# Performance work log

Hardware: AMD Instinct MI355X
Metric: run time of the kernel (lower is better)

The kernel has to match this reference:

```python
import jax, jax.numpy as jnp
import numpy as np

NUM_GROUPS = 32
EPS = 1e-5


def group_norm(x, scale, bias):
    # x: [B, C, L], normalize per (group, batch) over (C//G, L)
    B, C, L = x.shape
    G = NUM_GROUPS
    xg = x.reshape(B, G, C // G, L)
    mean = xg.mean(axis=(2, 3), keepdims=True)
    var = xg.var(axis=(2, 3), keepdims=True)
    xg = (xg - mean) * jax.lax.rsqrt(var + EPS)
    h = xg.reshape(B, C, L)
    return h * scale[None, :, None] + bias[None, :, None]


def setup_inputs() -> dict:
    key = jax.random.key(0)
    ks = jax.random.split(key, 8)
    B, C, L = 8, 512, 2048
    s = 1.0 / np.sqrt(C)
    return {
        "x": jax.random.normal(ks[0], (B, C, L), jnp.float32),
        "gn_scale": jnp.ones((C,), jnp.float32),
        "gn_bias": jnp.zeros((C,), jnp.float32),
        "wq": jax.random.normal(ks[1], (C, C), jnp.float32) * s,
        "bq": jnp.zeros((C,), jnp.float32),
        "wk": jax.random.normal(ks[2], (C, C), jnp.float32) * s,
        "bk": jnp.zeros((C,), jnp.float32),
        "wv": jax.random.normal(ks[3], (C, C), jnp.float32) * s,
        "bv": jnp.zeros((C,), jnp.float32),
        "wo": jax.random.normal(ks[4], (C, C), jnp.float32) * s,
        "bo": jnp.zeros((C,), jnp.float32),
    }


def reference(x, gn_scale, gn_bias, wq, bq, wk, bk, wv, bv, wo, bo):
    B, C, L = x.shape
    h = group_norm(x, gn_scale, gn_bias)  # [B, C, L]
    # 1x1 conv == per-position linear; produce [B, L, C] directly
    q = jnp.einsum('oc,bcl->blo', wq, h) + bq
    k = jnp.einsum('oc,bcl->blo', wk, h) + bk
    v = jnp.einsum('oc,bcl->blo', wv, h) + bv
    scale = jnp.asarray(C, x.dtype) ** -0.5
    w = jnp.einsum('bqc,bkc->bqk', q, k) * scale  # [B, L, L]
    w = jax.nn.softmax(w, axis=-1)
    a = jnp.einsum('bqk,bkc->bqc', w, v)  # [B, L, C]
    out = jnp.einsum('oc,blc->bol', wo, a) + bo[None, :, None]  # [B, C, L]
    return x + out
```

## Files before the change

kernel.cpp:

```cpp
#include <hip/hip_runtime.h>

typedef __attribute__((ext_vector_type(8))) _Float16 half8;
typedef __attribute__((ext_vector_type(4))) float floatx4;

#define AS1 __attribute__((address_space(1)))
#define AS3 __attribute__((address_space(3)))

__device__ __forceinline__ void async_load16(const void* g, void* l) {
  __builtin_amdgcn_global_load_lds((AS1 void*)(unsigned long long)g,
                                   (AS3 void*)(unsigned long long)l, 16, 0, 0);
}

template <int N>
__device__ __forceinline__ void wait_vm() {
  static_assert(N >= 0 && N <= 12, "extend wait_vm");
  if constexpr (N == 0) asm volatile("s_waitcnt vmcnt(0)" ::: "memory");
  else if constexpr (N == 1) asm volatile("s_waitcnt vmcnt(1)" ::: "memory");
  else if constexpr (N == 2) asm volatile("s_waitcnt vmcnt(2)" ::: "memory");
  else if constexpr (N == 3) asm volatile("s_waitcnt vmcnt(3)" ::: "memory");
  else if constexpr (N == 4) asm volatile("s_waitcnt vmcnt(4)" ::: "memory");
  else if constexpr (N == 5) asm volatile("s_waitcnt vmcnt(5)" ::: "memory");
  else if constexpr (N == 6) asm volatile("s_waitcnt vmcnt(6)" ::: "memory");
  else if constexpr (N == 7) asm volatile("s_waitcnt vmcnt(7)" ::: "memory");
  else if constexpr (N == 8) asm volatile("s_waitcnt vmcnt(8)" ::: "memory");
  else if constexpr (N == 9) asm volatile("s_waitcnt vmcnt(9)" ::: "memory");
  else if constexpr (N == 10) asm volatile("s_waitcnt vmcnt(10)" ::: "memory");
  else if constexpr (N == 11) asm volatile("s_waitcnt vmcnt(11)" ::: "memory");
  else asm volatile("s_waitcnt vmcnt(12)" ::: "memory");
}

__global__ __launch_bounds__(256) void gn_stats(const float* __restrict__ x,
                                                float* __restrict__ stats) {
  const int bg = blockIdx.x;
  const float4* p4 = (const float4*)(x + (long long)bg * 32768);
  const int t = threadIdx.x;
  float s = 0.f, ss = 0.f;
  for (int i = t; i < 8192; i += 256) {
    float4 v = p4[i];
    s += v.x + v.y + v.z + v.w;
    ss += v.x * v.x + v.y * v.y + v.z * v.z + v.w * v.w;
  }
#pragma unroll
  for (int off = 32; off; off >>= 1) { s += __shfl_down(s, off); ss += __shfl_down(ss, off); }
  __shared__ float rs[4], rss[4];
  if ((t & 63) == 0) { rs[t >> 6] = s; rss[t >> 6] = ss; }
  __syncthreads();
  if (t == 0) {
    s = rs[0] + rs[1] + rs[2] + rs[3];
    ss = rss[0] + rss[1] + rss[2] + rss[3];
    float mean = s * (1.f / 32768.f);
    float var = ss * (1.f / 32768.f) - mean * mean;
    stats[bg] = mean;
    stats[256 + bg] = rsqrtf(var + 1e-5f);
  }
}

__global__ __launch_bounds__(256) void gn_apply(const float* __restrict__ x,
                                                const float* __restrict__ stats,
                                                const float* __restrict__ gsc,
                                                const float* __restrict__ gbi,
                                                _Float16* __restrict__ ht) {
  __shared__ float tile[64][65];
  const int b = blockIdx.z, c0 = blockIdx.y * 64, l0 = blockIdx.x * 64;
  const int t = threadIdx.x, tr = t >> 6, tc = t & 63;
  const float* xb = x + ((long long)b * 512 + c0) * 2048 + l0;
#pragma unroll
  for (int p = 0; p < 16; ++p) {
    int row = tr + p * 4;
    tile[row][tc] = xb[(long long)row * 2048 + tc];
  }
  __syncthreads();
  const int c = c0 + tc;
  const int bg = b * 32 + (c >> 4);
  const float mean = stats[bg], rstd = stats[256 + bg];
  const float sc = gsc[c] * rstd;
  const float off = gbi[c] - mean * sc;
  _Float16* hb = ht + ((long long)b * 2048 + l0) * 512 + c0;
#pragma unroll
  for (int p = 0; p < 16; ++p) {
    int l = tr + p * 4;
    hb[(long long)l * 512 + tc] = (_Float16)(tile[tc][l] * sc + off);
  }
}

__global__ __launch_bounds__(256) void cast_w(const float* __restrict__ w0, const float* __restrict__ w1,
                                              const float* __restrict__ w2, const float* __restrict__ w3,
                                              const float* __restrict__ bq, const float* __restrict__ bk,
                                              _Float16* __restrict__ outw, float* __restrict__ bqk) {
  const long long i = (long long)blockIdx.x * 256 + threadIdx.x;
  if (blockIdx.x < 4096) {
    const int m = (int)(i >> 18);
    const int r = (int)(i & 262143);
    const float* w = (m == 0) ? w0 : (m == 1) ? w1 : (m == 2) ? w2 : w3;
    outw[i] = (_Float16)w[r];
  } else {
    const int j = (int)(i - 4096LL * 256);
    bqk[j] = (j < 512) ? bq[j] : bk[j - 512];
  }
}

template <int BM, int BN, int BIAS_MODE , int OUT_TYPE , bool RESIDUAL>
__global__ __launch_bounds__(512, 2) void gemm2p(
    const _Float16* __restrict__ A, long long sA, int lda,
    const _Float16* __restrict__ Bt, long long sB, int ldb,
    void* __restrict__ Cv, long long sC, int ldc,
    const float* __restrict__ bias,
    const float* __restrict__ resid, long long sR,
    float alpha, int K) {
  constexpr int ASZ = BM * 64, BSZ = BN * 64;
  constexpr int BUF = ASZ + BSZ;
  constexpr int RWA = BM / 16, RWB = BN / 16;
  constexpr int LA = RWA / 8, LB = RWB / 8;
  constexpr int L = 2 * LA + 2 * LB;
  constexpr int NMI = BM / 64, NNJ = BN / 128;
  __shared__ __align__(16) _Float16 ls[2 * BUF];

  const int tid = threadIdx.x;
  const int wave = tid >> 6, lane = tid & 63;
  const int wr = wave >> 2, wc = wave & 3;
  const int fm = lane & 15, q = lane >> 4;
  const int bz = blockIdx.x;
  const int m0 = blockIdx.y * BM, n0 = blockIdx.z * BN;
  A += (long long)bz * sA;
  Bt += (long long)bz * sB;

  const int srow = lane >> 3;
  const int schunk = ((lane & 7) ^ (srow & 7)) * 8;
  const _Float16* pA0 = A + (long long)(m0 + RWA * wave + srow) * lda + schunk;
  const _Float16* pA1 = pA0 + (long long)(BM / 2) * lda;
  const _Float16* pB0 = Bt + (long long)(n0 + RWB * wave + srow) * ldb + schunk;
  const _Float16* pB1 = pB0 + (long long)(BN / 2) * ldb;
  const int dA0 = RWA * wave * 64;
  const int dB0 = ASZ + RWB * wave * 64;

  const int c0 = (q ^ (fm & 7)) * 8;
  const int c1 = ((q + 4) ^ (fm & 7)) * 8;
  const int arow = wr * (BM / 4) + fm;
  const int brow = wc * (BN / 8) + fm;

  floatx4 acc[2][2][NMI][NNJ] = {};
  half8 af[NMI][2], bf0[NNJ][2], bf1[NNJ][2];

  const int NT = K >> 6;

  {
    _Float16* st = ls;
#pragma unroll
    for (int s = 0; s < LA; ++s) async_load16(pA0 + (long long)(8 * s) * lda, st + dA0 + s * 512);
#pragma unroll
    for (int s = 0; s < LB; ++s) async_load16(pB0 + (long long)(8 * s) * ldb, st + dB0 + s * 512);
#pragma unroll
    for (int s = 0; s < LB; ++s) async_load16(pB1 + (long long)(8 * s) * ldb, st + dB0 + BSZ / 2 + s * 512);
#pragma unroll
    for (int s = 0; s < LA; ++s) async_load16(pA1 + (long long)(8 * s) * lda, st + dA0 + ASZ / 2 + s * 512);
    pA0 += 64; pA1 += 64; pB0 += 64; pB1 += 64;
    wait_vm<0>();
  }

#define G8_READ_A(MH)                                                      \
  _Pragma("unroll") for (int mi = 0; mi < NMI; ++mi) {                     \
    const int r_ = (MH) * (BM / 2) + arow + 16 * mi;                       \
    af[mi][0] = *(const half8*)&cb[r_ * 64 + c0];                          \
    af[mi][1] = *(const half8*)&cb[r_ * 64 + c1];                          \
  }
#define G8_READ_B(NH, BF)                                                  \
  _Pragma("unroll") for (int nj = 0; nj < NNJ; ++nj) {                     \
    const int r_ = ASZ + ((NH) * (BN / 2) + brow + 16 * nj) * 64;          \
    BF[nj][0] = *(const half8*)&cb[r_ + c0];                               \
    BF[nj][1] = *(const half8*)&cb[r_ + c1];                               \
  }
#define G8_MFMA(MH, NH, BF)                                                \
  __builtin_amdgcn_s_setprio(1);                                           \
  _Pragma("unroll") for (int kk = 0; kk < 2; ++kk)                         \
  _Pragma("unroll") for (int mi = 0; mi < NMI; ++mi)                       \
  _Pragma("unroll") for (int nj = 0; nj < NNJ; ++nj)                       \
    acc[MH][NH][mi][nj] = __builtin_amdgcn_mfma_f32_16x16x32_f16(          \
        af[mi][kk], BF[nj][kk], acc[MH][NH][mi][nj], 0, 0, 0);             \
  __builtin_amdgcn_s_setprio(0);
#define G8_STAGE_A(PTR, OFF)                                               \
  _Pragma("unroll") for (int s = 0; s < LA; ++s)                           \
    async_load16(PTR + (long long)(8 * s) * lda, st + dA0 + (OFF) + s * 512);
#define G8_STAGE_B(PTR, OFF)                                               \
  _Pragma("unroll") for (int s = 0; s < LB; ++s)                           \
    async_load16(PTR + (long long)(8 * s) * ldb, st + dB0 + (OFF) + s * 512);

  for (int kt = 0; kt < NT - 1; ++kt) {
    const _Float16* cb = ls + (kt & 1) * BUF;
    _Float16* st = ls + ((kt + 1) & 1) * BUF;
    __builtin_amdgcn_s_barrier();
    G8_READ_A(0)
    G8_READ_B(0, bf0)
    G8_READ_B(1, bf1)
    G8_STAGE_A(pA0, 0)
    G8_STAGE_B(pB0, 0)
    G8_STAGE_B(pB1, BSZ / 2)
    G8_STAGE_A(pA1, ASZ / 2)
    pA0 += 64; pA1 += 64; pB0 += 64; pB1 += 64;
    wait_vm<L>();
    G8_MFMA(0, 0, bf0)
    G8_MFMA(0, 1, bf1)
    __builtin_amdgcn_s_barrier();
    G8_READ_A(1)
    wait_vm<LA>();
    G8_MFMA(1, 1, bf1)
    G8_MFMA(1, 0, bf0)
  }
  {
    const _Float16* cb = ls + ((NT - 1) & 1) * BUF;
    __builtin_amdgcn_s_barrier();
    G8_READ_A(0)
    G8_READ_B(0, bf0)
    G8_READ_B(1, bf1)
    wait_vm<0>();
    G8_MFMA(0, 0, bf0)
    G8_MFMA(0, 1, bf1)
    __builtin_amdgcn_s_barrier();
    G8_READ_A(1)
    G8_MFMA(1, 1, bf1)
    G8_MFMA(1, 0, bf0)
  }

#undef G8_READ_A
#undef G8_READ_B
#undef G8_MFMA
#undef G8_STAGE_A
#undef G8_STAGE_B

#pragma unroll
  for (int mh = 0; mh < 2; ++mh)
#pragma unroll
    for (int nh = 0; nh < 2; ++nh)
#pragma unroll
      for (int mi = 0; mi < NMI; ++mi)
#pragma unroll
        for (int nj = 0; nj < NNJ; ++nj) {
          const int rr0 = m0 + mh * (BM / 2) + wr * (BM / 4) + 16 * mi + 4 * q;
          const int cc = n0 + nh * (BN / 2) + wc * (BN / 8) + 16 * nj + fm;
#pragma unroll
          for (int t = 0; t < 4; ++t) {
            const int rr = rr0 + t;
            float v = acc[mh][nh][mi][nj][t] * alpha;
            if (BIAS_MODE == 1) v += bias[cc];
            if (BIAS_MODE == 2) v += bias[rr];
            if (RESIDUAL) v += resid[(long long)bz * sR + (long long)rr * ldc + cc];
            const long long off = (long long)bz * sC + (long long)rr * ldc + cc;
            if (OUT_TYPE == 0) ((float*)Cv)[off] = v;
            else ((_Float16*)Cv)[off] = (_Float16)v;
          }
        }
}

__global__ __launch_bounds__(256) void row_stats(const _Float16* __restrict__ S,
                                                 float2* __restrict__ rms) {
  const long long row = (long long)blockIdx.y * 2048 + blockIdx.x;
  const _Float16* p = S + row * 2048;
  const int t = threadIdx.x;
  union U { float4 f; _Float16 h[8]; } u;
  u.f = ((const float4*)p)[t];
  float v[8];
  float mx = -3e38f;
#pragma unroll
  for (int i = 0; i < 8; ++i) { v[i] = (float)u.h[i]; mx = fmaxf(mx, v[i]); }
#pragma unroll
  for (int off = 32; off; off >>= 1) mx = fmaxf(mx, __shfl_down(mx, off));
  __shared__ float red[4];
  if ((t & 63) == 0) red[t >> 6] = mx;
  __syncthreads();
  mx = fmaxf(fmaxf(red[0], red[1]), fmaxf(red[2], red[3]));
  float s = 0.f;
#pragma unroll
  for (int i = 0; i < 8; ++i) s += __expf(v[i] - mx);
#pragma unroll
  for (int off = 32; off; off >>= 1) s += __shfl_down(s, off);
  __syncthreads();
  if ((t & 63) == 0) red[t >> 6] = s;
  __syncthreads();
  if (t == 0) {
    s = red[0] + red[1] + red[2] + red[3];
    rms[blockIdx.y * 2048 + blockIdx.x] = make_float2(mx, 1.f / s);
  }
}

__global__ __launch_bounds__(512, 2) void gemm_pv(
    const _Float16* __restrict__ S, const float2* __restrict__ rms,
    const _Float16* __restrict__ Vt, _Float16* __restrict__ Out) {
  constexpr int BM = 128, BN = 256;
  constexpr int ASZ = BM * 64, BSZ = BN * 64, BUF = ASZ + BSZ;
  constexpr int LB = 2;
  constexpr int NMI = 2, NNJ = 2;
  constexpr int NT = 32;
  __shared__ __align__(16) _Float16 ls[2 * BUF];

  const int tid = threadIdx.x;
  const int wave = tid >> 6, lane = tid & 63;
  const int wr = wave >> 2, wc = wave & 3;
  const int fm = lane & 15, q = lane >> 4;
  const int bz = blockIdx.x;
  const int m0 = blockIdx.y * BM, n0 = blockIdx.z * BN;

  const int srow = lane >> 3;
  const int schunk = ((lane & 7) ^ (srow & 7)) * 8;
  const int rA0 = m0 + 8 * wave + srow;
  const float2 st0 = rms[bz * 2048 + rA0];
  const float2 st1 = rms[bz * 2048 + rA0 + 64];
  const _Float16* pA0 = S + (long long)bz * 4194304 + (long long)rA0 * 2048 + schunk;
  const _Float16* pA1 = pA0 + 64LL * 2048;
  const _Float16* pB0 = Vt + (long long)bz * 1048576 + (long long)(n0 + 16 * wave + srow) * 2048 + schunk;
  const _Float16* pB1 = pB0 + 128LL * 2048;
  const int dA0 = 8 * wave * 64;
  const int dB0 = ASZ + 16 * wave * 64;

  const int c0 = (q ^ (fm & 7)) * 8;
  const int c1 = ((q + 4) ^ (fm & 7)) * 8;
  const int arow = wr * (BM / 4) + fm;
  const int brow = wc * (BN / 8) + fm;

  floatx4 acc[2][2][NMI][NNJ] = {};
  half8 afx[2][NMI][2], bfx[2][NNJ][2];

#define PV_EXPW(DST, RA, MM, INV)                                          \
  { half8 pe_;                                                             \
    _Pragma("unroll") for (int e = 0; e < 8; ++e)                          \
      pe_[e] = (_Float16)(__expf((float)(RA)[e] - (MM)) * (INV));          \
    *(half8*)(DST) = pe_; }
#define PV_DMA_B(PTR, OFF)                                                 \
  _Pragma("unroll") for (int s = 0; s < LB; ++s)                           \
    async_load16(PTR + (long long)(8 * s) * 2048, stb + dB0 + (OFF) + s * 512);

  {
    _Float16* stb = ls;
    half8 ra0 = *(const half8*)pA0;
    half8 ra1 = *(const half8*)pA1;
    PV_DMA_B(pB0, 0)
    PV_DMA_B(pB1, BSZ / 2)
    PV_EXPW(&stb[dA0 + lane * 8], ra0, st0.x, st0.y)
    PV_EXPW(&stb[dA0 + ASZ / 2 + lane * 8], ra1, st1.x, st1.y)
    pA0 += 64; pA1 += 64; pB0 += 64; pB1 += 64;
    asm volatile("s_waitcnt vmcnt(0) lgkmcnt(0)" ::: "memory");
  }

  for (int kt = 0; kt < NT; ++kt) {
    const _Float16* cb = ls + (kt & 1) * BUF;
    _Float16* stb = ls + ((kt + 1) & 1) * BUF;
    __builtin_amdgcn_s_barrier();
#pragma unroll
    for (int mh = 0; mh < 2; ++mh)
#pragma unroll
      for (int mi = 0; mi < NMI; ++mi) {
        const int r_ = mh * (BM / 2) + arow + 16 * mi;
        afx[mh][mi][0] = *(const half8*)&cb[r_ * 64 + c0];
        afx[mh][mi][1] = *(const half8*)&cb[r_ * 64 + c1];
      }
#pragma unroll
    for (int nh = 0; nh < 2; ++nh)
#pragma unroll
      for (int nj = 0; nj < NNJ; ++nj) {
        const int r_ = ASZ + (nh * (BN / 2) + brow + 16 * nj) * 64;
        bfx[nh][nj][0] = *(const half8*)&cb[r_ + c0];
        bfx[nh][nj][1] = *(const half8*)&cb[r_ + c1];
      }
    half8 ra0, ra1;
    const bool more = (kt < NT - 1);
    if (more) {
      ra0 = *(const half8*)pA0;
      ra1 = *(const half8*)pA1;
      PV_DMA_B(pB0, 0)
      PV_DMA_B(pB1, BSZ / 2)
      pB0 += 64; pB1 += 64;
    }
    __builtin_amdgcn_s_setprio(1);
#pragma unroll
    for (int kk = 0; kk < 2; ++kk)
#pragma unroll
      for (int mh = 0; mh < 2; ++mh)
#pragma unroll
        for (int mi = 0; mi < NMI; ++mi)
#pragma unroll
          for (int nh = 0; nh < 2; ++nh)
#pragma unroll
            for (int nj = 0; nj < NNJ; ++nj)
              acc[mh][nh][mi][nj] = __builtin_amdgcn_mfma_f32_16x16x32_f16(
                  afx[mh][mi][kk], bfx[nh][nj][kk], acc[mh][nh][mi][nj], 0, 0, 0);
    __builtin_amdgcn_s_setprio(0);
    if (more) {
      PV_EXPW(&stb[dA0 + lane * 8], ra0, st0.x, st0.y)
      PV_EXPW(&stb[dA0 + ASZ / 2 + lane * 8], ra1, st1.x, st1.y)
      pA0 += 64; pA1 += 64;
    }
    asm volatile("s_waitcnt vmcnt(0) lgkmcnt(0)" ::: "memory");
  }
#undef PV_EXPW
#undef PV_DMA_B

#pragma unroll
  for (int mh = 0; mh < 2; ++mh)
#pragma unroll
    for (int nh = 0; nh < 2; ++nh)
#pragma unroll
      for (int mi = 0; mi < NMI; ++mi)
#pragma unroll
        for (int nj = 0; nj < NNJ; ++nj) {
          const int rr0 = m0 + mh * (BM / 2) + wr * (BM / 4) + 16 * mi + 4 * q;
          const int cc = n0 + nh * (BN / 2) + wc * (BN / 8) + 16 * nj + fm;
#pragma unroll
          for (int t = 0; t < 4; ++t) {
            const int rr = rr0 + t;
            Out[(long long)bz * 1048576 + (long long)rr * 512 + cc] =
                (_Float16)acc[mh][nh][mi][nj][t];
          }
        }
}

extern "C" void kernel_launch(void* const* d_in, const int* in_sizes, int n_in,
                              void* d_out, int out_size, void* d_ws, size_t ws_size,
                              hipStream_t stream) {
  const float* x = (const float*)d_in[0];
  const float* gsc = (const float*)d_in[1];
  const float* gbi = (const float*)d_in[2];
  const float* wq = (const float*)d_in[3];
  const float* bq = (const float*)d_in[4];
  const float* wk = (const float*)d_in[5];
  const float* bk = (const float*)d_in[6];
  const float* wv = (const float*)d_in[7];
  const float* bv = (const float*)d_in[8];
  const float* wo = (const float*)d_in[9];
  const float* bo = (const float*)d_in[10];
  float* out = (float*)d_out;

  char* ws = (char*)d_ws;
  float* stats = (float*)ws;
  float* bqk = (float*)(ws + 2048);
  _Float16* wbf = (_Float16*)(ws + 8192);
  _Float16* ht = wbf + 4 * 262144;
  const long long EB = 8LL * 2048 * 512;
  _Float16* qk = ht + EB;
  _Float16* vm = qk + 2 * EB;
  _Float16* Sb = vm + EB;
  _Float16* at = ht;
  float2* rms = (float2*)qk;

  gn_stats<<<256, 256, 0, stream>>>(x, stats);
  gn_apply<<<dim3(32, 8, 8), 256, 0, stream>>>(x, stats, gsc, gbi, ht);
  cast_w<<<4100, 256, 0, stream>>>(wq, wk, wv, wo, bq, bk, wbf, bqk);

  const float scale = 0.044194173824159216f;
  gemm2p<256, 256, 1, 1, false><<<dim3(8, 8, 4), 512, 0, stream>>>(
      ht, 1048576LL, 512, wbf, 0LL, 512, qk, 2097152LL, 1024, bqk, nullptr, 0LL, 1.f, 512);
  gemm2p<128, 256, 2, 1, false><<<dim3(8, 4, 8), 512, 0, stream>>>(
      wbf + 2 * 262144, 0LL, 512, ht, 1048576LL, 512, vm, 1048576LL, 2048, bv, nullptr, 0LL, 1.f, 512);
  gemm2p<256, 256, 0, 1, false><<<dim3(8, 8, 8), 512, 0, stream>>>(
      qk, 2097152LL, 1024, qk + 512, 2097152LL, 1024, Sb, 4194304LL, 2048, nullptr, nullptr, 0LL, scale, 512);
  row_stats<<<dim3(2048, 8), 256, 0, stream>>>(Sb, rms);
  gemm_pv<<<dim3(8, 16, 2), 512, 0, stream>>>(Sb, rms, vm, at);
  gemm2p<128, 256, 2, 0, true><<<dim3(8, 4, 8), 512, 0, stream>>>(
      wbf + 3 * 262144, 0LL, 512, at, 1048576LL, 512, out, 1048576LL, 2048, bo, x, 1048576LL, 1.f, 512);
}
```

Baseline: 277.2 us.

## Fuse group-norm stats/apply and compute softmax row stats in QK GEMM epilogue

Group norm now runs as one kernel. Each block computes its group's statistics, caches x as fp16 in LDS and writes the normalized, transposed output, so x is read once instead of twice. The separate row_stats pass over the score matrix is replaced by per-tile max/sum-exp partials computed in the QK^T GEMM epilogue, plus a small combine kernel, which avoids rereading S. The costs are a large LDS footprint in the group-norm kernel (about 64KB at 256 blocks, which limits parallelism) and extra epilogue work and synchronization in the score GEMM. Partials are written into the ht buffer, which is free at that point.

```diff
diff --git a/kernel.cpp b/kernel.cpp
--- a/kernel.cpp
+++ b/kernel.cpp
@@ -1,6 +1,7 @@
 #include <hip/hip_runtime.h>
 
 typedef __attribute__((ext_vector_type(8))) _Float16 half8;
+typedef __attribute__((ext_vector_type(4))) _Float16 half4;
 typedef __attribute__((ext_vector_type(4))) float floatx4;
 
 #define AS1 __attribute__((address_space(1)))
@@ -29,20 +30,30 @@
   else asm volatile("s_waitcnt vmcnt(12)" ::: "memory");
 }
 
-__global__ __launch_bounds__(256) void gn_stats(const float* __restrict__ x,
-                                                float* __restrict__ stats) {
+__global__ __launch_bounds__(256) void gn_fused(const float* __restrict__ x,
+                                                const float* __restrict__ gsc,
+                                                const float* __restrict__ gbi,
+                                                _Float16* __restrict__ ht) {
+  constexpr int STR = 2056;
+  __shared__ _Float16 xl[16 * STR];
+  __shared__ float rs[4], rss[4], mv[2], scs[16], ofs[16];
   const int bg = blockIdx.x;
+  const int b = bg >> 5, g = bg & 31;
   const float4* p4 = (const float4*)(x + (long long)bg * 32768);
   const int t = threadIdx.x;
   float s = 0.f, ss = 0.f;
   for (int i = t; i < 8192; i += 256) {
     float4 v = p4[i];
+    const int c = i >> 9, lq = (i & 511) << 2;
+    half4 pk;
+    pk[0] = (_Float16)v.x; pk[1] = (_Float16)v.y;
+    pk[2] = (_Float16)v.z; pk[3] = (_Float16)v.w;
+    *(half4*)&xl[c * STR + lq] = pk;
     s += v.x + v.y + v.z + v.w;
     ss += v.x * v.x + v.y * v.y + v.z * v.z + v.w * v.w;
   }
 #pragma unroll
   for (int off = 32; off; off >>= 1) { s += __shfl_down(s, off); ss += __shfl_down(ss, off); }
-  __shared__ float rs[4], rss[4];
   if ((t & 63) == 0) { rs[t >> 6] = s; rss[t >> 6] = ss; }
   __syncthreads();
   if (t == 0) {
@@ -50,36 +61,30 @@
     ss = rss[0] + rss[1] + rss[2] + rss[3];
     float mean = s * (1.f / 32768.f);
     float var = ss * (1.f / 32768.f) - mean * mean;
-    stats[bg] = mean;
-    stats[256 + bg] = rsqrtf(var + 1e-5f);
-  }
-}
-
-__global__ __launch_bounds__(256) void gn_apply(const float* __restrict__ x,
-                                                const float* __restrict__ stats,
-                                                const float* __restrict__ gsc,
-                                                const float* __restrict__ gbi,
-                                                _Float16* __restrict__ ht) {
-  __shared__ float tile[64][65];
-  const int b = blockIdx.z, c0 = blockIdx.y * 64, l0 = blockIdx.x * 64;
-  const int t = threadIdx.x, tr = t >> 6, tc = t & 63;
-  const float* xb = x + ((long long)b * 512 + c0) * 2048 + l0;
-#pragma unroll
-  for (int p = 0; p < 16; ++p) {
-    int row = tr + p * 4;
-    tile[row][tc] = xb[(long long)row * 2048 + tc];
+    mv[0] = mean; mv[1] = rsqrtf(var + 1e-5f);
   }
   __syncthreads();
-  const int c = c0 + tc;
-  const int bg = b * 32 + (c >> 4);
-  const float mean = stats[bg], rstd = stats[256 + bg];
-  const float sc = gsc[c] * rstd;
-  const float off = gbi[c] - mean * sc;
-  _Float16* hb = ht + ((long long)b * 2048 + l0) * 512 + c0;
-#pragma unroll
-  for (int p = 0; p < 16; ++p) {
-    int l = tr + p * 4;
-    hb[(long long)l * 512 + tc] = (_Float16)(tile[tc][l] * sc + off);
+  if (t < 16) {
+    const float sc = gsc[g * 16 + t] * mv[1];
+    scs[t] = sc;
+    ofs[t] = gbi[g * 16 + t] - mv[0] * sc;
+  }
+  __syncthreads();
+  const int l0 = t * 8;
+  half8 hv[16];
+#pragma unroll
+  for (int c = 0; c < 16; ++c) hv[c] = *(const half8*)&xl[c * STR + l0];
+  _Float16* dst0 = ht + ((long long)(b * 2048 + l0)) * 512 + g * 16;
+#pragma unroll
+  for (int j = 0; j < 8; ++j) {
+    half8 o0, o1;
+#pragma unroll
+    for (int c = 0; c < 8; ++c) o0[c] = (_Float16)((float)hv[c][j] * scs[c] + ofs[c]);
+#pragma unroll
+    for (int c = 0; c < 8; ++c) o1[c] = (_Float16)((float)hv[c + 8][j] * scs[c + 8] + ofs[c + 8]);
+    _Float16* dst = dst0 + (long long)j * 512;
+    *(half8*)dst = o0;
+    *(half8*)(dst + 8) = o1;
   }
 }
 
@@ -99,14 +104,15 @@
   }
 }
 
-template <int BM, int BN, int BIAS_MODE , int OUT_TYPE , bool RESIDUAL>
+template <int BM, int BN, int BIAS_MODE , int OUT_TYPE ,
+          bool RESIDUAL, bool STATS>
 __global__ __launch_bounds__(512, 2) void gemm2p(
     const _Float16* __restrict__ A, long long sA, int lda,
     const _Float16* __restrict__ Bt, long long sB, int ldb,
     void* __restrict__ Cv, long long sC, int ldc,
     const float* __restrict__ bias,
     const float* __restrict__ resid, long long sR,
-    float alpha, int K) {
+    float alpha, int K, float2* __restrict__ spart) {
   constexpr int ASZ = BM * 64, BSZ = BN * 64;
   constexpr int BUF = ASZ + BSZ;
   constexpr int RWA = BM / 16, RWB = BN / 16;
@@ -248,37 +254,57 @@
             else ((_Float16*)Cv)[off] = (_Float16)v;
           }
         }
-}
-
-__global__ __launch_bounds__(256) void row_stats(const _Float16* __restrict__ S,
-                                                 float2* __restrict__ rms) {
-  const long long row = (long long)blockIdx.y * 2048 + blockIdx.x;
-  const _Float16* p = S + row * 2048;
-  const int t = threadIdx.x;
-  union U { float4 f; _Float16 h[8]; } u;
-  u.f = ((const float4*)p)[t];
-  float v[8];
-  float mx = -3e38f;
-#pragma unroll
-  for (int i = 0; i < 8; ++i) { v[i] = (float)u.h[i]; mx = fmaxf(mx, v[i]); }
-#pragma unroll
-  for (int off = 32; off; off >>= 1) mx = fmaxf(mx, __shfl_down(mx, off));
-  __shared__ float red[4];
-  if ((t & 63) == 0) red[t >> 6] = mx;
-  __syncthreads();
-  mx = fmaxf(fmaxf(red[0], red[1]), fmaxf(red[2], red[3]));
-  float s = 0.f;
-#pragma unroll
-  for (int i = 0; i < 8; ++i) s += __expf(v[i] - mx);
-#pragma unroll
-  for (int off = 32; off; off >>= 1) s += __shfl_down(s, off);
-  __syncthreads();
-  if ((t & 63) == 0) red[t >> 6] = s;
-  __syncthreads();
-  if (t == 0) {
-    s = red[0] + red[1] + red[2] + red[3];
-    rms[blockIdx.y * 2048 + blockIdx.x] = make_float2(mx, 1.f / s);
-  }
+
+  if constexpr (STATS) {
+    float2* scr = (float2*)ls;
+    __syncthreads();
+#pragma unroll
+    for (int mh = 0; mh < 2; ++mh)
+#pragma unroll
+      for (int mi = 0; mi < NMI; ++mi)
+#pragma unroll
+        for (int t = 0; t < 4; ++t) {
+          const int r = mh * (BM / 2) + wr * (BM / 4) + mi * 16 + q * 4 + t;
+          const float v0 = (float)(_Float16)(acc[mh][0][mi][0][t] * alpha);
+          const float v1 = (float)(_Float16)(acc[mh][0][mi][1][t] * alpha);
+          const float v2 = (float)(_Float16)(acc[mh][1][mi][0][t] * alpha);
+          const float v3 = (float)(_Float16)(acc[mh][1][mi][1][t] * alpha);
+          const float m = fmaxf(fmaxf(v0, v1), fmaxf(v2, v3));
+          const float e = __expf(v0 - m) + __expf(v1 - m) + __expf(v2 - m) + __expf(v3 - m);
+          scr[r * 64 + wc * 16 + fm] = make_float2(m, e);
+        }
+    __syncthreads();
+    if (tid < BM) {
+      const int r = tid;
+      float M = -3e38f, E = 0.f;
+      const float4* scr4 = (const float4*)scr;
+      for (int k = 0; k < 32; ++k) {
+        const int jj = (r + k) & 31;
+        const float4 two = scr4[r * 32 + jj];
+        float nm = fmaxf(M, two.x);
+        E = E * __expf(M - nm) + two.y * __expf(two.x - nm);
+        M = nm;
+        nm = fmaxf(M, two.z);
+        E = E * __expf(M - nm) + two.w * __expf(two.z - nm);
+        M = nm;
+      }
+      spart[((long long)bz * 2048 + m0 + r) * 8 + blockIdx.z] = make_float2(M, E);
+    }
+  }
+}
+
+__global__ __launch_bounds__(256) void combine_stats(const float2* __restrict__ part,
+                                                     float2* __restrict__ rms) {
+  const int i = blockIdx.x * 256 + threadIdx.x;
+  float M = -3e38f, E = 0.f;
+#pragma unroll
+  for (int j = 0; j < 8; ++j) {
+    const float2 p = part[(long long)i * 8 + j];
+    const float nm = fmaxf(M, p.x);
+    E = E * __expf(M - nm) + p.y * __expf(p.x - nm);
+    M = nm;
+  }
+  rms[i] = make_float2(M, 1.f / E);
 }
 
 __global__ __launch_bounds__(512, 2) void gemm_pv(
@@ -428,7 +454,6 @@
   float* out = (float*)d_out;
 
   char* ws = (char*)d_ws;
-  float* stats = (float*)ws;
   float* bqk = (float*)(ws + 2048);
   _Float16* wbf = (_Float16*)(ws + 8192);
   _Float16* ht = wbf + 4 * 262144;
@@ -438,20 +463,20 @@
   _Float16* Sb = vm + EB;
   _Float16* at = ht;
   float2* rms = (float2*)qk;
-
-  gn_stats<<<256, 256, 0, stream>>>(x, stats);
-  gn_apply<<<dim3(32, 8, 8), 256, 0, stream>>>(x, stats, gsc, gbi, ht);
+  float2* spart = (float2*)ht;
+
+  gn_fused<<<256, 256, 0, stream>>>(x, gsc, gbi, ht);
   cast_w<<<4100, 256, 0, stream>>>(wq, wk, wv, wo, bq, bk, wbf, bqk);
 
   const float scale = 0.044194173824159216f;
-  gemm2p<256, 256, 1, 1, false><<<dim3(8, 8, 4), 512, 0, stream>>>(
-      ht, 1048576LL, 512, wbf, 0LL, 512, qk, 2097152LL, 1024, bqk, nullptr, 0LL, 1.f, 512);
-  gemm2p<128, 256, 2, 1, false><<<dim3(8, 4, 8), 512, 0, stream>>>(
-      wbf + 2 * 262144, 0LL, 512, ht, 1048576LL, 512, vm, 1048576LL, 2048, bv, nullptr, 0LL, 1.f, 512);
-  gemm2p<256, 256, 0, 1, false><<<dim3(8, 8, 8), 512, 0, stream>>>(
-      qk, 2097152LL, 1024, qk + 512, 2097152LL, 1024, Sb, 4194304LL, 2048, nullptr, nullptr, 0LL, scale, 512);
-  row_stats<<<dim3(2048, 8), 256, 0, stream>>>(Sb, rms);
+  gemm2p<256, 256, 1, 1, false, false><<<dim3(8, 8, 4), 512, 0, stream>>>(
+      ht, 1048576LL, 512, wbf, 0LL, 512, qk, 2097152LL, 1024, bqk, nullptr, 0LL, 1.f, 512, nullptr);
+  gemm2p<128, 256, 2, 1, false, false><<<dim3(8, 4, 8), 512, 0, stream>>>(
+      wbf + 2 * 262144, 0LL, 512, ht, 1048576LL, 512, vm, 1048576LL, 2048, bv, nullptr, 0LL, 1.f, 512, nullptr);
+  gemm2p<256, 256, 0, 1, false, true><<<dim3(8, 8, 8), 512, 0, stream>>>(
+      qk, 2097152LL, 1024, qk + 512, 2097152LL, 1024, Sb, 4194304LL, 2048, nullptr, nullptr, 0LL, scale, 512, spart);
+  combine_stats<<<64, 256, 0, stream>>>(spart, rms);
   gemm_pv<<<dim3(8, 16, 2), 512, 0, stream>>>(Sb, rms, vm, at);
-  gemm2p<128, 256, 2, 0, true><<<dim3(8, 4, 8), 512, 0, stream>>>(
-      wbf + 3 * 262144, 0LL, 512, at, 1048576LL, 512, out, 1048576LL, 2048, bo, x, 1048576LL, 1.f, 512);
-}
+  gemm2p<128, 256, 2, 0, true, false><<<dim3(8, 4, 8), 512, 0, stream>>>(
+      wbf + 3 * 262144, 0LL, 512, at, 1048576LL, 512, out, 1048576LL, 2048, bo, x, 1048576LL, 1.f, 512, nullptr);
+}
```

Result: no change. 278.5 us (+0.5%).

## Fuse group-norm statistics and apply into one kernel staging x in LDS

Applied to the files above, without the earlier changes.

Merges the separate group-norm statistics and normalize/transpose kernels into one kernel per (batch, group). It caches the group's input as fp16 in shared memory while reducing, then writes the normalized transposed fp16 output from shared memory. This removes a second full read of x from global memory and one kernel launch. In exchange, the big LDS footprint limits occupancy to one block per CU, and x is rounded to fp16 before the affine transform.

```diff
diff --git a/kernel.cpp b/kernel.cpp
--- a/kernel.cpp
+++ b/kernel.cpp
@@ -1,6 +1,7 @@
 #include <hip/hip_runtime.h>
 
 typedef __attribute__((ext_vector_type(8))) _Float16 half8;
+typedef __attribute__((ext_vector_type(4))) _Float16 half4;
 typedef __attribute__((ext_vector_type(4))) float floatx4;
 
 #define AS1 __attribute__((address_space(1)))
@@ -29,20 +30,30 @@
   else asm volatile("s_waitcnt vmcnt(12)" ::: "memory");
 }
 
-__global__ __launch_bounds__(256) void gn_stats(const float* __restrict__ x,
-                                                float* __restrict__ stats) {
+__global__ __launch_bounds__(256) void gn_fused(const float* __restrict__ x,
+                                                const float* __restrict__ gsc,
+                                                const float* __restrict__ gbi,
+                                                _Float16* __restrict__ ht) {
+  constexpr int STR = 2056;
+  __shared__ _Float16 xl[16 * STR];
+  __shared__ float rs[4], rss[4], mv[2], scs[16], ofs[16];
   const int bg = blockIdx.x;
+  const int b = bg >> 5, g = bg & 31;
   const float4* p4 = (const float4*)(x + (long long)bg * 32768);
   const int t = threadIdx.x;
   float s = 0.f, ss = 0.f;
   for (int i = t; i < 8192; i += 256) {
     float4 v = p4[i];
+    const int c = i >> 9, lq = (i & 511) << 2;
+    half4 pk;
+    pk[0] = (_Float16)v.x; pk[1] = (_Float16)v.y;
+    pk[2] = (_Float16)v.z; pk[3] = (_Float16)v.w;
+    *(half4*)&xl[c * STR + lq] = pk;
     s += v.x + v.y + v.z + v.w;
     ss += v.x * v.x + v.y * v.y + v.z * v.z + v.w * v.w;
   }
 #pragma unroll
   for (int off = 32; off; off >>= 1) { s += __shfl_down(s, off); ss += __shfl_down(ss, off); }
-  __shared__ float rs[4], rss[4];
   if ((t & 63) == 0) { rs[t >> 6] = s; rss[t >> 6] = ss; }
   __syncthreads();
   if (t == 0) {
@@ -50,36 +61,30 @@
     ss = rss[0] + rss[1] + rss[2] + rss[3];
     float mean = s * (1.f / 32768.f);
     float var = ss * (1.f / 32768.f) - mean * mean;
-    stats[bg] = mean;
-    stats[256 + bg] = rsqrtf(var + 1e-5f);
-  }
-}
-
-__global__ __launch_bounds__(256) void gn_apply(const float* __restrict__ x,
-                                                const float* __restrict__ stats,
-                                                const float* __restrict__ gsc,
-                                                const float* __restrict__ gbi,
-                                                _Float16* __restrict__ ht) {
-  __shared__ float tile[64][65];
-  const int b = blockIdx.z, c0 = blockIdx.y * 64, l0 = blockIdx.x * 64;
-  const int t = threadIdx.x, tr = t >> 6, tc = t & 63;
-  const float* xb = x + ((long long)b * 512 + c0) * 2048 + l0;
-#pragma unroll
-  for (int p = 0; p < 16; ++p) {
-    int row = tr + p * 4;
-    tile[row][tc] = xb[(long long)row * 2048 + tc];
-  }
-  __syncthreads();
-  const int c = c0 + tc;
-  const int bg = b * 32 + (c >> 4);
-  const float mean = stats[bg], rstd = stats[256 + bg];
-  const float sc = gsc[c] * rstd;
-  const float off = gbi[c] - mean * sc;
-  _Float16* hb = ht + ((long long)b * 2048 + l0) * 512 + c0;
-#pragma unroll
-  for (int p = 0; p < 16; ++p) {
-    int l = tr + p * 4;
-    hb[(long long)l * 512 + tc] = (_Float16)(tile[tc][l] * sc + off);
+    mv[0] = mean; mv[1] = rsqrtf(var + 1e-5f);
+  }
+  __syncthreads();
+  if (t < 16) {
+    const float sc = gsc[g * 16 + t] * mv[1];
+    scs[t] = sc;
+    ofs[t] = gbi[g * 16 + t] - mv[0] * sc;
+  }
+  __syncthreads();
+  const int l0 = t * 8;
+  half8 hv[16];
+#pragma unroll
+  for (int c = 0; c < 16; ++c) hv[c] = *(const half8*)&xl[c * STR + l0];
+  _Float16* dst0 = ht + ((long long)(b * 2048 + l0)) * 512 + g * 16;
+#pragma unroll
+  for (int j = 0; j < 8; ++j) {
+    half8 o0, o1;
+#pragma unroll
+    for (int c = 0; c < 8; ++c) o0[c] = (_Float16)((float)hv[c][j] * scs[c] + ofs[c]);
+#pragma unroll
+    for (int c = 0; c < 8; ++c) o1[c] = (_Float16)((float)hv[c + 8][j] * scs[c + 8] + ofs[c + 8]);
+    _Float16* dst = dst0 + (long long)j * 512;
+    *(half8*)dst = o0;
+    *(half8*)(dst + 8) = o1;
   }
 }
 
@@ -428,7 +433,6 @@
   float* out = (float*)d_out;
 
   char* ws = (char*)d_ws;
-  float* stats = (float*)ws;
   float* bqk = (float*)(ws + 2048);
   _Float16* wbf = (_Float16*)(ws + 8192);
   _Float16* ht = wbf + 4 * 262144;
@@ -439,8 +443,7 @@
   _Float16* at = ht;
   float2* rms = (float2*)qk;
 
-  gn_stats<<<256, 256, 0, stream>>>(x, stats);
-  gn_apply<<<dim3(32, 8, 8), 256, 0, stream>>>(x, stats, gsc, gbi, ht);
+  gn_fused<<<256, 256, 0, stream>>>(x, gsc, gbi, ht);
   cast_w<<<4100, 256, 0, stream>>>(wq, wk, wv, wo, bq, bk, wbf, bqk);
 
   const float scale = 0.044194173824159216f;
```

Result: slower. 287.0 us (+3.5%).
